# Performance work log

Hardware: AMD Instinct MI355X
Metric: run time of the kernel (lower is better)

Reference implementation:

```python
import jax, jax.numpy as jnp
import numpy as np
from jax import lax

B, N, D = 64, 499, 256          # batch, nodes(=seq_len), emb_size
NUM_P, NUM_Q, NUM_C = 10000, 2000, 10


def _seg_softmax(e, dst, n):
    # e: [E,H] edge scores, segment softmax over destination node
    m = jax.ops.segment_max(e, dst, num_segments=n)
    ex = jnp.exp(e - m[dst])
    s = jax.ops.segment_sum(ex, dst, num_segments=n)
    return ex / s[dst]


def gat_conv(x, src, dst, W, a_src, a_dst, b, concat):
    # x: [B,n,Fin], W: [Fin,H*Fo], a_src/a_dst: [H,Fo], b: [H*Fo] or [Fo]
    Bn, n, _ = x.shape
    H, Fo = a_src.shape
    h = (x @ W).reshape(Bn, n, H, Fo)
    es = jnp.einsum('bnhf,hf->bnh', h, a_src)
    ed = jnp.einsum('bnhf,hf->bnh', h, a_dst)
    e = jax.nn.leaky_relu(es[:, src] + ed[:, dst], 0.2)   # [B,E,H]
    alpha = jax.vmap(lambda eb: _seg_softmax(eb, dst, n))(e)
    msg = alpha[..., None] * h[:, src]                    # [B,E,H,Fo]
    out = jax.vmap(lambda mb: jax.ops.segment_sum(mb, dst, num_segments=n))(msg)
    out = out.reshape(Bn, n, H * Fo) if concat else out.mean(axis=2)
    return out + b


def lstm(xs, W_ih, W_hh, b_ih, b_hh):
    # xs: [B,S,I]; torch gate order i,f,g,o
    Bn = xs.shape[0]
    Hd = W_hh.shape[1]

    def step(carry, xt):
        h, c = carry
        g = xt @ W_ih.T + b_ih + h @ W_hh.T + b_hh
        i, f, gg, o = jnp.split(g, 4, axis=-1)
        c = jax.nn.sigmoid(f) * c + jax.nn.sigmoid(i) * jnp.tanh(gg)
        h = jax.nn.sigmoid(o) * jnp.tanh(c)
        return (h, c), h

    init = (jnp.zeros((Bn, Hd), xs.dtype), jnp.zeros((Bn, Hd), xs.dtype))
    _, hs = lax.scan(step, init, xs.transpose(1, 0, 2))
    return hs.transpose(1, 0, 2)


def _edges():
    # genr_edge_index(true_length-1=498): chain over nodes 0..497, then
    # PyG GATConv removes self-loops and adds them back for all 499 nodes.
    L = N - 1
    src, dst = [], []
    for i in range(L):
        for j in (i - 1, i + 1):
            if 0 <= j < L:
                src.append(i)
                dst.append(j)
    src += list(range(N))
    dst += list(range(N))
    return np.array(src, np.int32), np.array(dst, np.int32)


def setup_inputs() -> dict:
    key = jax.random.key(0)
    ks = jax.random.split(key, 30)
    f32 = jnp.float32

    def nrm(k, shape, s=0.05):
        return jax.random.normal(k, shape, dtype=f32) * s

    src, dst = _edges()
    inp = {
        'true_length': jnp.full((B,), N, dtype=jnp.int32),
        'p': jax.random.randint(ks[0], (B, N), 0, NUM_P + 1, dtype=jnp.int32),
        'q': jax.random.randint(ks[1], (B, N), 0, NUM_Q + 1, dtype=jnp.int32),
        'r': jax.random.randint(ks[2], (B, N), 0, 2, dtype=jnp.int32),
        'aff': jax.random.randint(ks[3], (B, N), 0, NUM_C + 1, dtype=jnp.int32),
        'q_next': jax.random.randint(ks[4], (B, N), 0, NUM_Q + 1, dtype=jnp.int32),
        'p_next': jax.random.randint(ks[5], (B, N), 0, NUM_P + 1, dtype=jnp.int32),
        'src': jnp.asarray(src),
        'dst': jnp.asarray(dst),
        'emb_p': nrm(ks[6], (NUM_P + 1, D), 1.0),
        'emb_q': nrm(ks[7], (NUM_Q + 1, D), 1.0),
        'emb_r': nrm(ks[8], (2, D), 1.0),
        'emb_aff': nrm(ks[9], (NUM_C + 1, D), 1.0),
        'W_affcat': nrm(ks[10], (2 * D, D)),
        'b_affcat': nrm(ks[11], (D,)),
        'W_g1': nrm(ks[12], (D, 8 * 128)),
        'a_src1': nrm(ks[13], (8, 128)),
        'a_dst1': nrm(ks[14], (8, 128)),
        'b_g1': nrm(ks[15], (8 * 128,)),
        'W_g2': nrm(ks[16], (8 * 128, D)),
        'a_src2': nrm(ks[17], (1, D)),
        'a_dst2': nrm(ks[18], (1, D)),
        'b_g2': nrm(ks[19], (D,)),
        'W_ih': nrm(ks[20], (4 * D, 4 * D)),
        'W_hh': nrm(ks[21], (4 * D, D)),
        'b_ih': nrm(ks[22], (4 * D,)),
        'b_hh': nrm(ks[23], (4 * D,)),
        'W_out': nrm(ks[24], (3 * D, 1)),
        'b_out': nrm(ks[25], (1,)),
    }
    return inp


def reference(true_length, p, q, r, aff, q_next, p_next, src, dst,
              emb_p, emb_q, emb_r, emb_aff, W_affcat, b_affcat,
              W_g1, a_src1, a_dst1, b_g1, W_g2, a_src2, a_dst2, b_g2,
              W_ih, W_hh, b_ih, b_hh, W_out, b_out):
    # eval mode: all dropouts are identity
    p_emb = emb_p[p]            # [B,N,D]
    q_emb = emb_q[q]
    r_emb = emb_r[r]
    qn_emb = emb_q[q_next]
    pn_emb = emb_p[p_next]
    aff_emb = emb_aff[aff]

    x = jnp.concatenate([p_emb, aff_emb], axis=-1) @ W_affcat + b_affcat
    x = jax.nn.elu(gat_conv(x, src, dst, W_g1, a_src1, a_dst1, b_g1, True))
    x = gat_conv(x, src, dst, W_g2, a_src2, a_dst2, b_g2, False)   # [B,N,D]

    seq = jnp.concatenate([p_emb, q_emb, r_emb, x], axis=-1)       # [B,N,4D]
    h = lstm(seq, W_ih, W_hh, b_ih, b_hh)                          # [B,N,D]
    y = jnp.concatenate([h, qn_emb, pn_emb], axis=-1) @ W_out + b_out
    return jax.nn.sigmoid(y)
```

## Files before the change

kernel.cpp:

```cpp
#include <hip/hip_runtime.h>
#include <hip/hip_bf16.h>

typedef unsigned int u32;
typedef unsigned short u16;

#define MTOT 31936
#define NN 499
#define BB 64

__device__ __forceinline__ float lo16(u32 u){ return __uint_as_float(u << 16); }
__device__ __forceinline__ float hi16(u32 u){ return __uint_as_float(u & 0xffff0000u); }
__device__ __forceinline__ float bf2f(u16 u){ return __uint_as_float(((u32)u) << 16); }
__device__ __forceinline__ u16 f2bf(float f){
  u32 x = __float_as_uint(f);
  u32 r = (x + 0x7fffu + ((x >> 16) & 1u)) >> 16;
  return (u16)r;
}
__device__ __forceinline__ float sigf(float x){ return 1.f / (1.f + __expf(-x)); }
__device__ __forceinline__ float tanh_(float x){ return 2.f * sigf(2.f * x) - 1.f; }
__device__ __forceinline__ float wred(float v){
  #pragma unroll
  for (int off = 32; off; off >>= 1) v += __shfl_down(v, off, 64);
  return v;
}

typedef __attribute__((ext_vector_type(2))) __bf16 bf16x2;

#if __has_builtin(__builtin_amdgcn_cvt_pk_bf16_f32)
__device__ __forceinline__ u32 pk2bf(float a, float b){
  union { bf16x2 v; u32 u; } r;
  r.v = __builtin_amdgcn_cvt_pk_bf16_f32(a, b);
  return r.u;
}
#else
__device__ __forceinline__ u32 pk2bf(float a, float b){
  return (u32)f2bf(a) | ((u32)f2bf(b) << 16);
}
#endif

typedef __attribute__((address_space(1))) void AS1void;
typedef __attribute__((address_space(3))) void AS3void;

typedef __attribute__((ext_vector_type(8))) short bfrag8;
typedef __attribute__((ext_vector_type(4))) float f4_t;
union FragU { uint4 u; bfrag8 s; };

__device__ __forceinline__ f4_t mfma16(FragU a, FragU b, f4_t c){
  return __builtin_amdgcn_mfma_f32_16x16x32_bf16(a.s, b.s, c, 0, 0, 0);
}

template <typename AP>
__device__ __forceinline__ void gemm_core3(int K32, const uint4* __restrict__ Bpack,
                                           int ntBase, f4_t (&acc)[4][2], AP aaddr){
  __shared__ __align__(16) uint4 As[2][256];
  const int tid = threadIdx.x;
  const int wave = tid >> 6, lane = tid & 63;
  const uint4* Bp0 = Bpack + ((size_t)ntBase * K32) * 64 + lane;
  const uint4* Bp1 = Bp0 + (size_t)K32 * 64;
  int buf = 0;
  for (int kt = 0; kt < K32; kt++){
    FragU b0, b1;
    b0.u = Bp0[kt * 64];
    b1.u = Bp1[kt * 64];
    __builtin_amdgcn_global_load_lds((AS1void*)aaddr(kt),
                                     (AS3void*)&As[buf][wave * 64], 16, 0, 0);
    __syncthreads();
    FragU a0, a1, a2, a3;
    a0.u = As[buf][lane];
    a1.u = As[buf][64 + lane];
    a2.u = As[buf][128 + lane];
    a3.u = As[buf][192 + lane];
    acc[0][0] = mfma16(a0, b0, acc[0][0]); acc[0][1] = mfma16(a0, b1, acc[0][1]);
    acc[1][0] = mfma16(a1, b0, acc[1][0]); acc[1][1] = mfma16(a1, b1, acc[1][1]);
    acc[2][0] = mfma16(a2, b0, acc[2][0]); acc[2][1] = mfma16(a2, b1, acc[2][1]);
    acc[3][0] = mfma16(a3, b0, acc[3][0]); acc[3][1] = mfma16(a3, b1, acc[3][1]);
    buf ^= 1;
  }
}

__global__ __launch_bounds__(256) void k_packE(const float* __restrict__ in,
                                               u16* __restrict__ out, int n4){
  int i = blockIdx.x * 256 + threadIdx.x;
  if (i >= n4) return;
  float4 v = ((const float4*)in)[i];
  uint2 o; o.x = pk2bf(v.x, v.y); o.y = pk2bf(v.z, v.w);
  ((uint2*)out)[i] = o;
}

__global__ __launch_bounds__(256) void k_packB(const float* __restrict__ W, u16* __restrict__ out,
                                               int K, int N, int trans){
  int c = blockIdx.x * 256 + threadIdx.x;
  int K32 = K >> 5;
  int total = (N >> 4) * K32 * 64;
  if (c >= total) return;
  int l = c & 63;
  int rem = c >> 6;
  int kt = rem % K32, nt = rem / K32;
  int n = nt * 16 + (l & 15);
  int kb = kt * 32 + (l >> 4) * 8;
  u32 ov[4];
  #pragma unroll
  for (int j2 = 0; j2 < 4; j2++){
    int k = kb + j2 * 2;
    float f0 = trans ? W[(size_t)n * K + k]     : W[(size_t)k * N + n];
    float f1 = trans ? W[(size_t)n * K + k + 1] : W[(size_t)(k + 1) * N + n];
    ov[j2] = pk2bf(f0, f1);
  }
  uint4 o; o.x = ov[0]; o.y = ov[1]; o.z = ov[2]; o.w = ov[3];
  *(uint4*)(out + (size_t)c * 8) = o;
}

__global__ void k_csr(const int* __restrict__ src, const int* __restrict__ dst, int E,
                      int* __restrict__ deg, int* __restrict__ insrc){
  int tid = threadIdx.x;
  for (int i = tid; i < NN; i += 256) deg[i] = 0;
  for (int i = tid; i < NN * 4; i += 256) insrc[i] = 0;
  __syncthreads();
  for (int e = tid; e < E; e += 256){
    int d = dst[e];
    int slot = atomicAdd(&deg[d], 1);
    if (slot < 4) insrc[d * 4 + slot] = src[e];
  }
}

__global__ __launch_bounds__(256) void k_affcat_m(
    const u16* __restrict__ emb_pb, const u16* __restrict__ emb_ab,
    const int* __restrict__ p, const int* __restrict__ aff,
    const uint4* __restrict__ Bpack, const float* __restrict__ bias, u16* __restrict__ Cb){
  const int tid = threadIdx.x;
  const int mBase = blockIdx.x * 64, nBase = blockIdx.y * 128;
  const int ls = tid & 63;
  const int gm = mBase + (tid >> 6) * 16 + (ls & 15);
  const int kqoff = (ls >> 4) * 8;
  const u16* rp = emb_pb + (size_t)p[gm] * 256 + kqoff;
  const u16* ra = emb_ab + (size_t)aff[gm] * 256 + kqoff;
  f4_t acc[4][2] = {};
  gemm_core3(16, Bpack, blockIdx.y * 8 + ((tid >> 6) << 1), acc, [&](int kt) -> const void* {
    int kb = kt * 32;
    return (kb < 256) ? (const void*)(rp + kb) : (const void*)(ra + kb - 256);
  });
  const int wave = tid >> 6, lane = tid & 63;
  const int rb = (lane >> 4) << 2;
  const int cbase = nBase + wave * 32 + (lane & 15);
  float b0 = bias[cbase], b1 = bias[cbase + 16];
  #pragma unroll
  for (int i = 0; i < 4; i++)
    #pragma unroll
    for (int r = 0; r < 4; r++){
      int row = mBase + i * 16 + rb + r;
      Cb[(size_t)row * 256 + cbase]      = f2bf(acc[i][0][r] + b0);
      Cb[(size_t)row * 256 + cbase + 16] = f2bf(acc[i][1][r] + b1);
    }
}

__global__ __launch_bounds__(256) void k_h1_m(const u16* __restrict__ A,
                                              const uint4* __restrict__ Bpack,
                                              u16* __restrict__ Cb){
  const int tid = threadIdx.x;
  const int mBase = blockIdx.x * 64, nBase = blockIdx.y * 128;
  const int ls = tid & 63;
  const int gm = mBase + (tid >> 6) * 16 + (ls & 15);
  const u16* ra = A + (size_t)gm * 256 + (ls >> 4) * 8;
  f4_t acc[4][2] = {};
  gemm_core3(8, Bpack, blockIdx.y * 8 + ((tid >> 6) << 1), acc, [&](int kt) -> const void* {
    return (const void*)(ra + kt * 32);
  });
  const int wave = tid >> 6, lane = tid & 63;
  const int rb = (lane >> 4) << 2;
  const int cbase = nBase + wave * 32 + (lane & 15);
  #pragma unroll
  for (int i = 0; i < 4; i++)
    #pragma unroll
    for (int r = 0; r < 4; r++){
      int row = mBase + i * 16 + rb + r;
      Cb[(size_t)row * 1024 + cbase]      = f2bf(acc[i][0][r]);
      Cb[(size_t)row * 1024 + cbase + 16] = f2bf(acc[i][1][r]);
    }
}

__global__ __launch_bounds__(256) void k_h2_m(const u16* __restrict__ A,
                                              const uint4* __restrict__ Bpack,
                                              float* __restrict__ C){
  const int tid = threadIdx.x;
  const int mBase = blockIdx.x * 64, nBase = blockIdx.y * 128;
  const int ls = tid & 63;
  const int gm = mBase + (tid >> 6) * 16 + (ls & 15);
  const u16* ra = A + (size_t)gm * 1024 + (ls >> 4) * 8;
  f4_t acc[4][2] = {};
  gemm_core3(32, Bpack, blockIdx.y * 8 + ((tid >> 6) << 1), acc, [&](int kt) -> const void* {
    return (const void*)(ra + kt * 32);
  });
  const int wave = tid >> 6, lane = tid & 63;
  const int rb = (lane >> 4) << 2;
  const int cbase = nBase + wave * 32 + (lane & 15);
  #pragma unroll
  for (int i = 0; i < 4; i++)
    #pragma unroll
    for (int r = 0; r < 4; r++){
      int row = mBase + i * 16 + rb + r;
      C[(size_t)row * 256 + cbase]      = acc[i][0][r];
      C[(size_t)row * 256 + cbase + 16] = acc[i][1][r];
    }
}

__global__ __launch_bounds__(256) void k_gates_m(
    const u16* __restrict__ emb_pb, const u16* __restrict__ emb_qb, const u16* __restrict__ emb_rb,
    const int* __restrict__ p, const int* __restrict__ q, const int* __restrict__ r,
    const u16* __restrict__ x2b, const uint4* __restrict__ Bpack,
    const float* __restrict__ bih, const float* __restrict__ bhh, u16* __restrict__ Cb){
  const int tid = threadIdx.x;
  const int mBase = blockIdx.x * 64, nBase = blockIdx.y * 128;
  const int ls = tid & 63;
  const int gm = mBase + (tid >> 6) * 16 + (ls & 15);
  const int kqoff = (ls >> 4) * 8;
  const u16* s0 = emb_pb + (size_t)p[gm] * 256 + kqoff;
  const u16* s1 = emb_qb + (size_t)q[gm] * 256 + kqoff;
  const u16* s2 = emb_rb + (size_t)r[gm] * 256 + kqoff;
  const u16* s3 = x2b + (size_t)gm * 256 + kqoff;
  f4_t acc[4][2] = {};
  gemm_core3(32, Bpack, blockIdx.y * 8 + ((tid >> 6) << 1), acc, [&](int kt) -> const void* {
    int kb = kt * 32;
    int seg = kb >> 8, ko = kb & 255;
    const u16* s = (seg == 0) ? s0 : ((seg == 1) ? s1 : ((seg == 2) ? s2 : s3));
    return (const void*)(s + ko);
  });
  const int wave = tid >> 6, lane = tid & 63;
  const int rb = (lane >> 4) << 2;
  const int cbase = nBase + wave * 32 + (lane & 15);
  float b0 = bih[cbase] + bhh[cbase];
  float b1 = bih[cbase + 16] + bhh[cbase + 16];
  #pragma unroll
  for (int i = 0; i < 4; i++)
    #pragma unroll
    for (int r2 = 0; r2 < 4; r2++){
      int row = mBase + i * 16 + rb + r2;
      Cb[(size_t)row * 1024 + cbase]      = f2bf(acc[i][0][r2] + b0);
      Cb[(size_t)row * 1024 + cbase + 16] = f2bf(acc[i][1][r2] + b1);
    }
}

__global__ __launch_bounds__(256) void k_repack2(const u16* __restrict__ gates,
                                                 u16* __restrict__ G2){
  __shared__ __align__(16) u16 staged[1024];
  const int tid = threadIdx.x;
  const size_t m = blockIdx.x;
  const u32* row32 = (const u32*)(gates + m * 1024);
  ((u32*)staged)[tid]       = row32[tid];
  ((u32*)staged)[tid + 256] = row32[tid + 256];
  __syncthreads();
  if (tid < 128){
    const int w = tid >> 4, uc = tid & 15;
    u32 vw[4];
    #pragma unroll
    for (int j = 0; j < 4; j++){
      const int P = j >> 1, glo = (j & 1) * 2;
      const u16 lo = staged[glo * 256 + w * 32 + P * 16 + uc];
      const u16 hi = staged[(glo + 1) * 256 + w * 32 + P * 16 + uc];
      vw[j] = (u32)lo | ((u32)hi << 16);
    }
    uint4 o; o.x = vw[0]; o.y = vw[1]; o.z = vw[2]; o.w = vw[3];
    *(uint4*)(G2 + (m * 128 + (size_t)tid) * 8) = o;
  }
}

__global__ __launch_bounds__(256) void k_esed(
    const u16* __restrict__ hb, const float* __restrict__ hf,
    const float* __restrict__ asrc, const float* __restrict__ adst,
    float* __restrict__ es, float* __restrict__ ed, int Hm1, int Fo){
  int w = blockIdx.x * 4 + (threadIdx.x >> 6);
  int lane = threadIdx.x & 63;
  int h = w & Hm1;
  size_t base = (size_t)w * Fo;
  float s = 0.f, d = 0.f;
  for (int f = lane; f < Fo; f += 64){
    float hv = hb ? bf2f(hb[base + f]) : hf[base + f];
    s += hv * asrc[h * Fo + f];
    d += hv * adst[h * Fo + f];
  }
  s = wred(s); d = wred(d);
  if (!lane){ es[w] = s; ed[w] = d; }
}

__global__ __launch_bounds__(256) void k_gatagg(
    const u16* __restrict__ hb, const float* __restrict__ hf,
    const float* __restrict__ es, const float* __restrict__ ed,
    const int* __restrict__ deg, const int* __restrict__ insrc,
    const float* __restrict__ bias, u16* __restrict__ outb, float* __restrict__ outf,
    int H, int foShift, int HFo, int do_elu){
  int m = blockIdx.x;
  int b = m / NN;
  int n = m - b * NN;
  int dg = deg[n];
  int s0 = insrc[n * 4 + 0];
  int s1 = insrc[n * 4 + 1];
  int s2 = insrc[n * 4 + 2];
  int rowBase = b * NN;
  for (int c = threadIdx.x; c < HFo; c += 256){
    int h = c >> foShift;
    float edv = ed[(size_t)m * H + h];
    float sc0 = es[(size_t)(rowBase + s0) * H + h] + edv;
    sc0 = (sc0 >= 0.f) ? sc0 : 0.2f * sc0;
    float sc1 = 0.f, sc2 = 0.f, mx = sc0;
    if (dg > 1){ sc1 = es[(size_t)(rowBase + s1) * H + h] + edv; sc1 = (sc1 >= 0.f) ? sc1 : 0.2f * sc1; mx = fmaxf(mx, sc1); }
    if (dg > 2){ sc2 = es[(size_t)(rowBase + s2) * H + h] + edv; sc2 = (sc2 >= 0.f) ? sc2 : 0.2f * sc2; mx = fmaxf(mx, sc2); }
    float e0 = __expf(sc0 - mx), e1 = 0.f, e2 = 0.f;
    if (dg > 1) e1 = __expf(sc1 - mx);
    if (dg > 2) e2 = __expf(sc2 - mx);
    float inv = 1.f / (e0 + e1 + e2);
    size_t c0 = (size_t)(rowBase + s0) * HFo + c;
    float acc = e0 * (hb ? bf2f(hb[c0]) : hf[c0]);
    if (dg > 1){ size_t c1 = (size_t)(rowBase + s1) * HFo + c; acc += e1 * (hb ? bf2f(hb[c1]) : hf[c1]); }
    if (dg > 2){ size_t c2 = (size_t)(rowBase + s2) * HFo + c; acc += e2 * (hb ? bf2f(hb[c2]) : hf[c2]); }
    acc *= inv;
    float o = acc + bias[c];
    if (do_elu) o = (o > 0.f) ? o : (__expf(o) - 1.f);
    if (outb) outb[(size_t)m * HFo + c] = f2bf(o);
    else      outf[(size_t)m * HFo + c] = o;
  }
}

#define WREG 32
#define WLDS 17
__global__ __launch_bounds__(512)
__attribute__((amdgpu_waves_per_eu(2, 2)))
void k_lstm(const u16* __restrict__ g2,
            const uint4* __restrict__ bph,
            float* __restrict__ h_all){
  __shared__ __align__(16) uint4 wlds[8][WLDS][64];
  __shared__ __align__(16) u16 hsh[2][256];
  const int b = blockIdx.x, tid = threadIdx.x;
  const int w = tid >> 6, lane = tid & 63;
  const int uc = lane & 15, oct = lane >> 4;
  if (tid < 128) ((u32*)hsh[1])[tid] = 0u;

  uint4 wreg[WREG];
  #pragma unroll
  for (int kc = 0; kc < 8; kc++)
    #pragma unroll
    for (int g = 0; g < 3; g++)
      wreg[kc * 3 + g] = bph[(size_t)(((g * 16 + w * 2) * 8 + kc) * 64) + lane];
  wreg[24] = bph[(size_t)(((48 + w * 2) * 8) * 64) + lane];
  #pragma unroll
  for (int kc = 1; kc < 8; kc++)
    wreg[24 + kc] = bph[(size_t)(((32 + w * 2 + 1) * 8 + kc) * 64) + lane];
  #pragma unroll
  for (int kc = 0; kc < 8; kc++){
    wlds[w][kc][lane]     = bph[(size_t)(((w * 2 + 1) * 8 + kc) * 64) + lane];
    wlds[w][8 + kc][lane] = bph[(size_t)(((16 + w * 2 + 1) * 8 + kc) * 64) + lane];
  }
  wlds[w][16][lane] = bph[(size_t)(((32 + w * 2 + 1) * 8) * 64) + lane];

  const uint4* sp = bph + (size_t)(((48 + w * 2) * 8) * 64) + lane;

  const uint4* g0p = (const uint4*)g2 + (size_t)b * NN * 128 + w * 16 + uc;
  uint4 G0q = *g0p;
  g0p += 128;

  const size_t hofs0 = ((size_t)b * NN) * 256 + (size_t)w * 32 + uc;
  float cst[2] = {0.f, 0.f};

  uint4 wstr[6];
  #pragma unroll
  for (int s = 0; s < 6; s++) wstr[s] = sp[(s + 1) * 64];
  __syncthreads();

  #pragma unroll 1
  for (int n = 0; n < NN; n++){
    const char* hrd = (const char*)hsh[(n + 1) & 1];
    char* hwr = (char*)hsh[n & 1];
    f4_t acc[8] = {};
    #pragma unroll
    for (int ph = 0; ph < 16; ph++){
      const int P = ph >> 3, kc = ph & 7;
      FragU a;
      a.u = *(const uint4*)(hrd + (u32)(kc * 64 + oct * 16));
      #pragma unroll
      for (int g = 0; g < 4; g++){
        FragU bb;
        if (P == 0){
          if (g < 3)            bb.u = wreg[kc * 3 + g];
          else if (kc == 0)     bb.u = wreg[24];
          else                  bb.u = wstr[(ph - 1) % 6];
        } else {
          if (g == 0)           bb.u = wlds[w][kc][lane];
          else if (g == 1)      bb.u = wlds[w][8 + kc][lane];
          else if (g == 2)      bb.u = (kc == 0) ? wlds[w][16][lane] : wreg[24 + kc];
          else                  bb.u = wstr[(ph - 1) % 6];
        }
        acc[P * 4 + g] = mfma16(a, bb, acc[P * 4 + g]);
      }
      if (ph >= 1 && ph <= 9)
        wstr[(ph + 5) % 6] = sp[(ph + 6) * 64];
    }
    #pragma unroll
    for (int s = 0; s < 6; s++) wstr[s] = sp[(s + 1) * 64];
    float hv2[2];
    #pragma unroll
    for (int P = 0; P < 2; P++){
      float gv[4];
      #pragma unroll
      for (int g = 0; g < 4; g++){
        const int wi = P * 2 + (g >> 1);
        const u32 uw = (wi == 0) ? G0q.x : (wi == 1) ? G0q.y : (wi == 2) ? G0q.z : G0q.w;
        gv[g] = acc[P * 4 + g][0] + ((g & 1) ? hi16(uw) : lo16(uw));
      }
      const float cv = sigf(gv[1]) * cst[P] + sigf(gv[0]) * tanh_(gv[2]);
      cst[P] = cv;
      hv2[P] = sigf(gv[3]) * tanh_(cv);
    }
    if (oct == 0){
      #pragma unroll
      for (int P = 0; P < 2; P++){
        const int u = w * 32 + P * 16 + uc;
        *(u16*)(hwr + u * 2) = f2bf(hv2[P]);
        h_all[hofs0 + (size_t)n * 256 + P * 16] = hv2[P];
      }
    }
    if (n + 1 < NN){
      G0q = *g0p;
      g0p += 128;
    }
    asm volatile("s_waitcnt lgkmcnt(0)" ::: "memory");
    __builtin_amdgcn_s_barrier();
    __builtin_amdgcn_sched_barrier(0);
  }
}

__global__ __launch_bounds__(256) void k_out(const float* __restrict__ h_all,
    const float* __restrict__ emb_q, const float* __restrict__ emb_p,
    const int* __restrict__ qn, const int* __restrict__ pn,
    const float* __restrict__ Wo, const float* __restrict__ bo, float* __restrict__ y){
  int m = blockIdx.x * 4 + (threadIdx.x >> 6);
  int lane = threadIdx.x & 63;
  const float* hr = h_all + (size_t)m * 256;
  const float* rq = emb_q + (size_t)qn[m] * 256;
  const float* rp = emb_p + (size_t)pn[m] * 256;
  float acc = 0.f;
  #pragma unroll
  for (int f = 0; f < 256; f += 64){
    int d = f + lane;
    acc += hr[d] * Wo[d];
    acc += rq[d] * Wo[256 + d];
    acc += rp[d] * Wo[512 + d];
  }
  acc = wred(acc);
  if (!lane) y[m] = sigf(acc + bo[0]);
}

extern "C" void kernel_launch(void* const* d_in, const int* in_sizes, int n_in,
                              void* d_out, int out_size, void* d_ws, size_t ws_size,
                              hipStream_t stream){
  (void)n_in; (void)out_size; (void)ws_size;
  const int* p    = (const int*)d_in[1];
  const int* q    = (const int*)d_in[2];
  const int* r    = (const int*)d_in[3];
  const int* aff  = (const int*)d_in[4];
  const int* qn   = (const int*)d_in[5];
  const int* pn   = (const int*)d_in[6];
  const int* src  = (const int*)d_in[7];
  const int* dst  = (const int*)d_in[8];
  const float* emb_p  = (const float*)d_in[9];
  const float* emb_q  = (const float*)d_in[10];
  const float* emb_r  = (const float*)d_in[11];
  const float* emb_aff= (const float*)d_in[12];
  const float* W_aff  = (const float*)d_in[13];
  const float* b_aff  = (const float*)d_in[14];
  const float* W_g1   = (const float*)d_in[15];
  const float* a_s1   = (const float*)d_in[16];
  const float* a_d1   = (const float*)d_in[17];
  const float* b_g1   = (const float*)d_in[18];
  const float* W_g2   = (const float*)d_in[19];
  const float* a_s2   = (const float*)d_in[20];
  const float* a_d2   = (const float*)d_in[21];
  const float* b_g2   = (const float*)d_in[22];
  const float* W_ih   = (const float*)d_in[23];
  const float* W_hh   = (const float*)d_in[24];
  const float* b_ih   = (const float*)d_in[25];
  const float* b_hh   = (const float*)d_in[26];
  const float* W_out  = (const float*)d_in[27];
  const float* b_out  = (const float*)d_in[28];
  const int E = in_sizes[7];

  char* ws = (char*)d_ws;
  size_t off = 0;
  auto alloc = [&](size_t bytes){ size_t ret = off; off += (bytes + 255) & ~(size_t)255; return ret; };
  size_t o_bigA = alloc((size_t)MTOT * 1024 * 2);
  size_t o_bigB = alloc((size_t)MTOT * 1024 * 2);
  size_t o_buf3 = alloc((size_t)MTOT * 256 * 4);
  size_t o_es1 = alloc((size_t)MTOT * 8 * 4);
  size_t o_ed1 = alloc((size_t)MTOT * 8 * 4);
  size_t o_es2 = alloc((size_t)MTOT * 4);
  size_t o_ed2 = alloc((size_t)MTOT * 4);
  size_t o_whh = alloc((size_t)32768 * 16);
  size_t o_deg = alloc(512 * 4);
  size_t o_ins = alloc((size_t)NN * 4 * 4);
  size_t o_bpih  = alloc((size_t)131072 * 16);
  size_t o_bpg1  = alloc((size_t)32768 * 16);
  size_t o_bpg2  = alloc((size_t)32768 * 16);
  size_t o_bpaff = alloc((size_t)16384 * 16);
  size_t o_ebp = alloc((size_t)10001 * 256 * 2);
  size_t o_ebq = alloc((size_t)2001 * 256 * 2);
  size_t o_ebr = alloc((size_t)2 * 256 * 2);
  size_t o_eba = alloc((size_t)11 * 256 * 2);

  u16*   h1    = (u16*)(ws + o_bigA);
  u16*   gates = (u16*)(ws + o_bigA);
  u16*   g1out = (u16*)(ws + o_bigB);
  u16*   x2b   = (u16*)(ws + o_bigB);
  u16*   G2    = (u16*)(ws + o_bigB);
  u16*   x0b   = (u16*)(ws + o_buf3);
  float* h2    = (float*)(ws + o_buf3);
  float* h_all = (float*)(ws + o_buf3);
  float* es1   = (float*)(ws + o_es1);
  float* ed1   = (float*)(ws + o_ed1);
  float* es2   = (float*)(ws + o_es2);
  float* ed2   = (float*)(ws + o_ed2);
  u16*   bphh  = (u16*)(ws + o_whh);
  int*   degp  = (int*)(ws + o_deg);
  int*   insp  = (int*)(ws + o_ins);
  u16*   bpih  = (u16*)(ws + o_bpih);
  u16*   bpg1  = (u16*)(ws + o_bpg1);
  u16*   bpg2  = (u16*)(ws + o_bpg2);
  u16*   bpaff = (u16*)(ws + o_bpaff);
  u16*   ebp   = (u16*)(ws + o_ebp);
  u16*   ebq   = (u16*)(ws + o_ebq);
  u16*   ebr   = (u16*)(ws + o_ebr);
  u16*   eba   = (u16*)(ws + o_eba);

  k_csr<<<1, 256, 0, stream>>>(src, dst, E, degp, insp);
  k_packB<<<128, 256, 0, stream>>>(W_hh, bphh, 256, 1024, 1);
  k_packB<<<512, 256, 0, stream>>>(W_ih, bpih, 1024, 1024, 1);
  k_packB<<<128, 256, 0, stream>>>(W_g1, bpg1, 256, 1024, 0);
  k_packB<<<128, 256, 0, stream>>>(W_g2, bpg2, 1024, 256, 0);
  k_packB<<<64, 256, 0, stream>>>(W_aff, bpaff, 512, 256, 0);
  k_packE<<<2501, 256, 0, stream>>>(emb_p, ebp, 10001 * 64);
  k_packE<<<501, 256, 0, stream>>>(emb_q, ebq, 2001 * 64);
  k_packE<<<1, 256, 0, stream>>>(emb_r, ebr, 2 * 64);
  k_packE<<<3, 256, 0, stream>>>(emb_aff, eba, 11 * 64);

  k_affcat_m<<<dim3(NN, 2), 256, 0, stream>>>(ebp, eba, p, aff,
                                              (const uint4*)bpaff, b_aff, x0b);
  k_h1_m<<<dim3(NN, 8), 256, 0, stream>>>(x0b, (const uint4*)bpg1, h1);
  k_esed<<<(MTOT * 8) / 4, 256, 0, stream>>>(h1, nullptr, a_s1, a_d1, es1, ed1, 7, 128);
  k_gatagg<<<MTOT, 256, 0, stream>>>(h1, nullptr, es1, ed1, degp, insp, b_g1,
                                     g1out, nullptr, 8, 7, 1024, 1);
  k_h2_m<<<dim3(NN, 2), 256, 0, stream>>>(g1out, (const uint4*)bpg2, h2);
  k_esed<<<MTOT / 4, 256, 0, stream>>>(nullptr, h2, a_s2, a_d2, es2, ed2, 0, 256);
  k_gatagg<<<MTOT, 256, 0, stream>>>(nullptr, h2, es2, ed2, degp, insp, b_g2,
                                     x2b, nullptr, 1, 8, 256, 0);
  k_gates_m<<<dim3(NN, 8), 256, 0, stream>>>(ebp, ebq, ebr, p, q, r, x2b,
                                             (const uint4*)bpih, b_ih, b_hh, gates);
  k_repack2<<<MTOT, 256, 0, stream>>>(gates, G2);
  k_lstm<<<BB, 512, 0, stream>>>(G2, (const uint4*)bphh, h_all);
  k_out<<<MTOT / 4, 256, 0, stream>>>(h_all, emb_q, emb_p, qn, pn, W_out, b_out, (float*)d_out);
}
```

Baseline: 1.485 ms.

## Stream LSTM second-half weights from global via register ring instead of LDS

The LSTM recurrent kernel no longer stages part of W_hh in LDS. It keeps the first 32 fragments (P=0, all four gates) in registers and streams all 32 P=1 fragments from global or L2 each timestep through an 8-slot register prefetch ring, two k-chunks ahead. This removes the LDS reads and the per-wave weight LDS footprint and simplifies fragment selection. The cost is much more global or cache traffic on the serial recurrence path, plus added latency exposure per step.

```diff
diff --git a/kernel.cpp b/kernel.cpp
--- a/kernel.cpp
+++ b/kernel.cpp
@@ -319,38 +319,25 @@
   }
 }
 
-#define WREG 32
-#define WLDS 17
 __global__ __launch_bounds__(512)
 __attribute__((amdgpu_waves_per_eu(2, 2)))
 void k_lstm(const u16* __restrict__ g2,
             const uint4* __restrict__ bph,
             float* __restrict__ h_all){
-  __shared__ __align__(16) uint4 wlds[8][WLDS][64];
   __shared__ __align__(16) u16 hsh[2][256];
   const int b = blockIdx.x, tid = threadIdx.x;
   const int w = tid >> 6, lane = tid & 63;
   const int uc = lane & 15, oct = lane >> 4;
   if (tid < 128) ((u32*)hsh[1])[tid] = 0u;
 
-  uint4 wreg[WREG];
+  uint4 wreg[32];
   #pragma unroll
   for (int kc = 0; kc < 8; kc++)
     #pragma unroll
-    for (int g = 0; g < 3; g++)
-      wreg[kc * 3 + g] = bph[(size_t)(((g * 16 + w * 2) * 8 + kc) * 64) + lane];
-  wreg[24] = bph[(size_t)(((48 + w * 2) * 8) * 64) + lane];
-  #pragma unroll
-  for (int kc = 1; kc < 8; kc++)
-    wreg[24 + kc] = bph[(size_t)(((32 + w * 2 + 1) * 8 + kc) * 64) + lane];
-  #pragma unroll
-  for (int kc = 0; kc < 8; kc++){
-    wlds[w][kc][lane]     = bph[(size_t)(((w * 2 + 1) * 8 + kc) * 64) + lane];
-    wlds[w][8 + kc][lane] = bph[(size_t)(((16 + w * 2 + 1) * 8 + kc) * 64) + lane];
-  }
-  wlds[w][16][lane] = bph[(size_t)(((32 + w * 2 + 1) * 8) * 64) + lane];
-
-  const uint4* sp = bph + (size_t)(((48 + w * 2) * 8) * 64) + lane;
+    for (int g = 0; g < 4; g++)
+      wreg[kc * 4 + g] = bph[(size_t)(((g * 16 + w * 2) * 8 + kc) * 64) + lane];
+
+  const uint4* pB = bph + (size_t)(((w * 2 + 1) * 8) * 64) + lane;
 
   const uint4* g0p = (const uint4*)g2 + (size_t)b * NN * 128 + w * 16 + uc;
   uint4 G0q = *g0p;
@@ -359,9 +346,9 @@
   const size_t hofs0 = ((size_t)b * NN) * 256 + (size_t)w * 32 + uc;
   float cst[2] = {0.f, 0.f};
 
-  uint4 wstr[6];
-  #pragma unroll
-  for (int s = 0; s < 6; s++) wstr[s] = sp[(s + 1) * 64];
+  uint4 ring[8];
+  #pragma unroll
+  for (int s = 0; s < 8; s++) ring[s] = pB[(s & 3) * 8192 + (s >> 2) * 64];
   __syncthreads();
 
   #pragma unroll 1
@@ -370,30 +357,25 @@
     char* hwr = (char*)hsh[n & 1];
     f4_t acc[8] = {};
     #pragma unroll
-    for (int ph = 0; ph < 16; ph++){
-      const int P = ph >> 3, kc = ph & 7;
+    for (int kc = 0; kc < 8; kc++){
       FragU a;
       a.u = *(const uint4*)(hrd + (u32)(kc * 64 + oct * 16));
       #pragma unroll
       for (int g = 0; g < 4; g++){
-        FragU bb;
-        if (P == 0){
-          if (g < 3)            bb.u = wreg[kc * 3 + g];
-          else if (kc == 0)     bb.u = wreg[24];
-          else                  bb.u = wstr[(ph - 1) % 6];
-        } else {
-          if (g == 0)           bb.u = wlds[w][kc][lane];
-          else if (g == 1)      bb.u = wlds[w][8 + kc][lane];
-          else if (g == 2)      bb.u = (kc == 0) ? wlds[w][16][lane] : wreg[24 + kc];
-          else                  bb.u = wstr[(ph - 1) % 6];
-        }
-        acc[P * 4 + g] = mfma16(a, bb, acc[P * 4 + g]);
+        FragU bb; bb.u = wreg[kc * 4 + g];
+        acc[g] = mfma16(a, bb, acc[g]);
       }
-      if (ph >= 1 && ph <= 9)
-        wstr[(ph + 5) % 6] = sp[(ph + 6) * 64];
-    }
-    #pragma unroll
-    for (int s = 0; s < 6; s++) wstr[s] = sp[(s + 1) * 64];
+      #pragma unroll
+      for (int g = 0; g < 4; g++){
+        FragU bb; bb.u = ring[(kc * 4 + g) & 7];
+        acc[4 + g] = mfma16(a, bb, acc[4 + g]);
+      }
+      #pragma unroll
+      for (int g = 0; g < 4; g++){
+        const int c2 = (kc + 2) & 7;
+        ring[(c2 * 4 + g) & 7] = pB[g * 8192 + c2 * 64];
+      }
+    }
     float hv2[2];
     #pragma unroll
     for (int P = 0; P < 2; P++){
```

New measurement: 2.703 ms. 1.82x slower.
